# Kernel tuning notes

Measured on AMD Instinct MI355X. Metric: run time of the kernel, lower is better.

The kernel has to match this reference:

```python
import jax, jax.numpy as jnp
import numpy as np

OUT_K = 7  # out_kernel


def setup_inputs() -> dict:
    key = jax.random.key(0)
    k = jax.random.split(key, 12)
    b, cin, h, w = 2, 256, 64, 64
    C, pd = 64, 4          # out_channels, pos_dim
    qc = C - pd            # channels produced by conv_q/k/v
    s = 0.05
    f32 = jnp.float32
    return {
        "x":    jax.random.normal(k[0], (b, cin, h, w), f32),
        "Wq":   jax.random.normal(k[1], (qc, cin), f32) * s,
        "bq":   jax.random.normal(k[2], (qc,), f32) * s,
        "Wk":   jax.random.normal(k[3], (qc, cin), f32) * s,
        "bk":   jax.random.normal(k[4], (qc,), f32) * s,
        "Wv":   jax.random.normal(k[5], (qc, cin), f32) * s,
        "bv":   jax.random.normal(k[6], (qc,), f32) * s,
        "Wp":   jax.random.normal(k[7], (pd, 2), f32) * s,
        "bp":   jax.random.normal(k[8], (pd,), f32) * s,
        "Wout": jax.random.normal(k[9], (C, C, OUT_K, OUT_K), f32) * s,
        "bout": jax.random.normal(k[10], (C,), f32) * s,
    }


def reference(x, Wq, bq, Wk, bk, Wv, bv, Wp, bp, Wout, bout):
    b, cin, h, w = x.shape
    C = Wout.shape[0]  # out_channels
    dt = x.dtype

    # positional encoding: hw_pose is (row_index, col_index) grids -> 1x1 conv to pos_dim chans
    rows = jnp.broadcast_to(jnp.arange(h, dtype=dt)[:, None], (h, w))
    cols = jnp.broadcast_to(jnp.arange(w, dtype=dt)[None, :], (h, w))
    grid = jnp.stack([rows, cols], axis=0)                      # (2,h,w)
    pos = jnp.einsum('oc,chw->ohw', Wp, grid) + bp[:, None, None]  # (pd,h,w)
    pos = jnp.broadcast_to(pos[None], (b,) + pos.shape)         # (b,pd,h,w)

    def conv1x1(W, bias):
        return jnp.einsum('bchw,oc->bohw', x, W) + bias[None, :, None, None]

    qs = jnp.concatenate([conv1x1(Wq, bq), pos], axis=1)        # (b,C,h,w)
    ks = jnp.concatenate([conv1x1(Wk, bk), pos], axis=1)
    vs = jnp.concatenate([conv1x1(Wv, bv), pos], axis=1)

    hw = h * w
    qsf = qs.transpose(0, 2, 3, 1).reshape(b, hw, C)            # (b,hw,C)
    ksf = ks.reshape(b, C, hw)                                  # (b,C,hw)
    vsf = vs.transpose(0, 2, 3, 1)                              # (b,h,w,C)

    qk = jnp.einsum('bnc,bcm->bnm', qsf, ksf) / jnp.sqrt(jnp.asarray(C, dt))
    diag = jnp.arange(hw)
    qk = qk.at[:, diag, diag].set(0.0)                          # zero diagonal BEFORE softmax
    attn = jax.nn.softmax(qk, axis=-1).reshape(b, h, w, h, w)

    # 7x7 clamped neighborhood gather (replaces the 49-iteration python loop)
    r = OUT_K // 2
    offs = jnp.arange(-r, r + 1)
    hi = jnp.clip(jnp.arange(h)[:, None] + offs[None, :], 0, h - 1)  # (h,7)
    wi = jnp.clip(jnp.arange(w)[:, None] + offs[None, :], 0, w - 1)  # (w,7)
    ii = jnp.arange(h)[:, None, None, None]
    jj = jnp.arange(w)[None, :, None, None]
    hk = hi[:, None, :, None]
    wk = wi[None, :, None, :]
    attn_loc = attn[:, ii, jj, hk, wk]                          # (b,h,w,7,7)
    v_loc = vsf[:, hk, wk, :]                                   # (b,h,w,7,7,C)

    qkv = attn_loc[..., None] * v_loc                           # (b,h,w,7,7,C)
    # con_out: kernel=7, stride=7 over a 7x7 patch == full contraction
    out = jnp.einsum('bhwklc,ockl->bhwo', qkv, Wout) + bout     # (b,h,w,C)
    out = jax.nn.relu(out)
    return out.transpose(0, 3, 1, 2)                            # (b,C,h,w)
```

## Files before the change

kernel.cpp:

```cpp
#include <hip/hip_runtime.h>
#include <math.h>

#define NTAP 49

typedef short bf16x8 __attribute__((ext_vector_type(8)));
typedef float f32x4  __attribute__((ext_vector_type(4)));

__device__ __forceinline__ float b2f(ushort u) {
    return __uint_as_float(((unsigned)u) << 16);
}
__device__ __forceinline__ ushort f2b(float f) {
    unsigned u = __float_as_uint(f);
    return (ushort)((u + 0x7FFFu + ((u >> 16) & 1u)) >> 16);
}
__device__ __forceinline__ int iclamp(int x) { return min(max(x, 0), 63); }

#define LOG2E 1.44269504f
#define S2    (0.125f * LOG2E)

#define WTB_OFF 0u
#define WAH_OFF 401408u
#define WAL_OFF 499712u
#define QH_OFF  598016u
#define KH_OFF  1646592u
#define VH_OFF  2695168u
#define LP_OFF  3743744u
#define ST_OFF  4005888u

__global__ __launch_bounds__(256) void k_prep(
    const float* __restrict__ Wout,
    const float* __restrict__ Wq, const float* __restrict__ Wk, const float* __restrict__ Wv,
    ushort* __restrict__ Wtb, ushort* __restrict__ WAh, ushort* __restrict__ WAl,
    int* __restrict__ ST)
{
    int idx = blockIdx.x * 256 + threadIdx.x;
    if (idx < 4) ST[idx] = 0;
    if (idx < 192 * 256) {
        int m = idx >> 8, c = idx & 255;
        int mat = m >> 6, o = m & 63;
        float v = 0.f;
        if (o < 60) {
            const float* Wm = (mat == 0) ? Wq : (mat == 1) ? Wk : Wv;
            v = Wm[o * 256 + c];
        }
        ushort h = f2b(v);
        WAh[idx] = h;
        WAl[idx] = f2b(v - b2f(h));
    }
    if (idx < 64 * 64 * NTAP) {
        int o   = idx / (64 * NTAP);
        int rem = idx - o * (64 * NTAP);
        int c   = rem / NTAP;
        int kl  = rem - c * NTAP;
        Wtb[(o * NTAP + kl) * 64 + c] = f2b(Wout[idx]);
    }
}

__device__ __forceinline__ float get_mhat(const int* ST, int b) {
    float q2 = __int_as_float(ST[b]);
    float k2 = __int_as_float(ST[2 + b]);
    return 0.125f * sqrtf(q2) * sqrtf(k2) + 1.0f;
}

__global__ __launch_bounds__(512, 2) void k_qkv(
    const float* __restrict__ x,
    const ushort* __restrict__ WAh, const ushort* __restrict__ WAl,
    const float* __restrict__ bq, const float* __restrict__ bk, const float* __restrict__ bv,
    const float* __restrict__ Wp, const float* __restrict__ bp,
    ushort* __restrict__ QKV, int* __restrict__ ST)
{
    __shared__ ushort Xh[32 * 256];
    __shared__ ushort Xl[32 * 256];
    __shared__ ushort Wshl[192 * 64];
    __shared__ float  sqL[64];
    int bid = blockIdx.x;
    int b   = bid >> 7;
    int n0  = (bid & 127) * 32;
    int t   = threadIdx.x;
    int w    = t >> 6;
    int L    = t & 63;
    int lrow = L & 15, lk = L >> 4;

    if (t < 64) sqL[t] = 0.f;
    {
        int p  = t & 31;
        int cg = t >> 5;
        #pragma unroll
        for (int it = 0; it < 2; ++it) {
            int cgi = cg + it * 16;
            float v[8];
            #pragma unroll
            for (int e = 0; e < 8; ++e)
                v[e] = x[((size_t)(b * 256 + cgi * 8 + e) << 12) + n0 + p];
            bf16x8 hi, lo;
            #pragma unroll
            for (int e = 0; e < 8; ++e) {
                ushort h = f2b(v[e]);
                hi[e] = (short)h;
                lo[e] = (short)f2b(v[e] - b2f(h));
            }
            int off = p * 256 + ((cgi * 8) ^ ((p & 7) * 8));
            *(bf16x8*)(Xh + off) = hi;
            *(bf16x8*)(Xl + off) = lo;
        }
    }

    int pxh = w >> 2;
    int ob  = (w & 3) * 48;
    int px  = pxh * 16 + lrow;

    f32x4 acc[3] = {{0,0,0,0},{0,0,0,0},{0,0,0,0}};

    for (int c8 = 0; c8 < 8; ++c8) {
        __syncthreads();
        #pragma unroll
        for (int s = 0; s < 3; ++s) {
            int g_idx = t + s * 512;
            int och = g_idx >> 3, g = g_idx & 7;
            const ushort* src = (g < 4) ? WAh : WAl;
            bf16x8 val = *(const bf16x8*)(src + och * 256 + c8 * 32 + (g & 3) * 8);
            *(bf16x8*)((char*)Wshl + och * 128 + ((g * 16) ^ ((och & 7) << 4))) = val;
        }
        __syncthreads();

        int cidx = (c8 * 4 + lk) * 8;
        int o0 = px * 256 + (cidx ^ ((px & 7) * 8));
        bf16x8 ah = *(const bf16x8*)(Xh + o0);
        bf16x8 al = *(const bf16x8*)(Xl + o0);
        #pragma unroll
        for (int c = 0; c < 3; ++c) {
            int och = ob + c * 16 + lrow;
            const char* wb = (const char*)Wshl + och * 128;
            int swz = (och & 7) << 4;
            bf16x8 bh = *(const bf16x8*)(wb + ((lk * 16) ^ swz));
            bf16x8 bl = *(const bf16x8*)(wb + (((4 + lk) * 16) ^ swz));
            acc[c] = __builtin_amdgcn_mfma_f32_16x16x32_bf16(al, bh, acc[c], 0, 0, 0);
            acc[c] = __builtin_amdgcn_mfma_f32_16x16x32_bf16(ah, bl, acc[c], 0, 0, 0);
            acc[c] = __builtin_amdgcn_mfma_f32_16x16x32_bf16(ah, bh, acc[c], 0, 0, 0);
        }
    }

    float s_q[4] = {0,0,0,0}, s_k[4] = {0,0,0,0};
    #pragma unroll
    for (int c = 0; c < 3; ++c) {
        int och = ob + c * 16 + lrow;
        int mat = och >> 6;
        int o   = och & 63;
        const float* bm = (mat == 0) ? bq : (mat == 1) ? bk : bv;
        ushort* Ob = QKV + (size_t)mat * 524288;
        if (o < 60) {
            float bias = bm[o];
            #pragma unroll
            for (int e = 0; e < 4; ++e) {
                int n = n0 + pxh * 16 + lk * 4 + e;
                float v = acc[c][e] + bias;
                Ob[((size_t)((b << 12) + n)) * 64 + o] = f2b(v);
                if (mat == 0) s_q[e] = fmaf(v, v, s_q[e]);
                else if (mat == 1) s_k[e] = fmaf(v, v, s_k[e]);
            }
        } else {
            int po = o - 60;
            float w0 = Wp[2 * po], w1 = Wp[2 * po + 1], b0 = bp[po];
            #pragma unroll
            for (int e = 0; e < 4; ++e) {
                int n = n0 + pxh * 16 + lk * 4 + e;
                float fi = (float)(n >> 6), fj = (float)(n & 63);
                float pv = fmaf(w0, fi, fmaf(w1, fj, b0));
                Ob[((size_t)((b << 12) + n)) * 64 + o] = f2b(pv);
                if (mat == 0) s_q[e] = fmaf(pv, pv, s_q[e]);
                else if (mat == 1) s_k[e] = fmaf(pv, pv, s_k[e]);
            }
        }
    }
    #pragma unroll
    for (int off = 1; off < 16; off <<= 1) {
        #pragma unroll
        for (int e = 0; e < 4; ++e) {
            s_q[e] += __shfl_xor(s_q[e], off, 64);
            s_k[e] += __shfl_xor(s_k[e], off, 64);
        }
    }
    if (lrow == 0) {
        #pragma unroll
        for (int e = 0; e < 4; ++e) {
            int pix = pxh * 16 + lk * 4 + e;
            atomicAdd(&sqL[pix],      s_q[e]);
            atomicAdd(&sqL[32 + pix], s_k[e]);
        }
    }
    __syncthreads();
    if (t < 32) {
        float q2 = sqL[t], k2 = sqL[32 + t];
        #pragma unroll
        for (int off = 1; off < 32; off <<= 1) {
            q2 = fmaxf(q2, __shfl_xor(q2, off, 64));
            k2 = fmaxf(k2, __shfl_xor(k2, off, 64));
        }
        if (t == 0) {
            atomicMax(ST + b,     __float_as_int(q2));
            atomicMax(ST + 2 + b, __float_as_int(k2));
        }
    }
}

__global__ __launch_bounds__(512, 2) void k_stats(
    const ushort* __restrict__ QH, const ushort* __restrict__ KH,
    const int* __restrict__ ST, float* __restrict__ Lp)
{
    __shared__ ushort Ks[2][128 * 64];
    int bid = blockIdx.x;
    int ks  = bid & 7;
    int r   = bid >> 3;
    int b   = r >> 5;
    int n0  = (r & 31) * 128;
    int ck0 = ks * 512;
    float bse = -get_mhat(ST, b) * LOG2E;

    int t = threadIdx.x;
    int w = t >> 6, L = t & 63;
    int lrow = L & 15, lk = L >> 4;

    size_t qbase = ((size_t)((b << 12) + n0 + w * 16 + lrow)) * 64 + lk * 8;
    bf16x8 a0 = *(const bf16x8*)(QH + qbase);
    bf16x8 a1 = *(const bf16x8*)(QH + qbase + 32);

    #pragma unroll
    for (int gi = 0; gi < 2; ++gi) {
        int g = t + gi * 512;
        int u = g >> 3, c8 = g & 7;
        bf16x8 val = *(const bf16x8*)(KH + ((size_t)((b << 12) + ck0 + u)) * 64 + c8 * 8);
        *(bf16x8*)((char*)Ks[0] + u * 128 + ((c8 * 16) ^ ((u & 7) << 4))) = val;
    }

    float rs0 = 0.f, rs1 = 0.f, rs2 = 0.f, rs3 = 0.f;

    for (int c = 0; c < 4; ++c) {
        bf16x8 st0, st1;
        int u0 = t >> 3, c80 = t & 7;
        int u1 = (t + 512) >> 3, c81 = t & 7;
        bool pf = (c + 1) < 4;
        if (pf) {
            st0 = *(const bf16x8*)(KH + ((size_t)((b << 12) + ck0 + (c + 1) * 128 + u0)) * 64 + c80 * 8);
            st1 = *(const bf16x8*)(KH + ((size_t)((b << 12) + ck0 + (c + 1) * 128 + u1)) * 64 + c81 * 8);
        }
        __syncthreads();
        const char* kb = (const char*)Ks[c & 1];
        #pragma unroll
        for (int kg = 0; kg < 8; ++kg) {
            int u = kg * 16 + lrow;
            int swz = (u & 7) << 4;
            bf16x8 b0 = *(const bf16x8*)(kb + u * 128 + ((lk * 16) ^ swz));
            bf16x8 b1 = *(const bf16x8*)(kb + u * 128 + ((64 + lk * 16) ^ swz));
            f32x4 z = {0.f, 0.f, 0.f, 0.f};
            z = __builtin_amdgcn_mfma_f32_16x16x32_bf16(a0, b0, z, 0, 0, 0);
            z = __builtin_amdgcn_mfma_f32_16x16x32_bf16(a1, b1, z, 0, 0, 0);
            rs0 += exp2f(fmaf(z[0], S2, bse));
            rs1 += exp2f(fmaf(z[1], S2, bse));
            rs2 += exp2f(fmaf(z[2], S2, bse));
            rs3 += exp2f(fmaf(z[3], S2, bse));
        }
        if (pf) {
            char* kn = (char*)Ks[(c + 1) & 1];
            *(bf16x8*)(kn + u0 * 128 + ((c80 * 16) ^ ((u0 & 7) << 4))) = st0;
            *(bf16x8*)(kn + u1 * 128 + ((c81 * 16) ^ ((u1 & 7) << 4))) = st1;
        }
    }
    #pragma unroll
    for (int off = 1; off < 16; off <<= 1) {
        rs0 += __shfl_xor(rs0, off, 64);
        rs1 += __shfl_xor(rs1, off, 64);
        rs2 += __shfl_xor(rs2, off, 64);
        rs3 += __shfl_xor(rs3, off, 64);
    }
    if (lrow == 0) {
        float* dst = Lp + ((size_t)(ks * 2 + b) << 12) + n0 + w * 16 + lk * 4;
        dst[0] = rs0; dst[1] = rs1; dst[2] = rs2; dst[3] = rs3;
    }
}

__global__ __launch_bounds__(512, 2) void k_out(
    const ushort* __restrict__ QH, const ushort* __restrict__ KH,
    const ushort* __restrict__ VH, const ushort* __restrict__ Wtb,
    const float* __restrict__ Lp, const int* __restrict__ ST,
    const float* __restrict__ bout, float* __restrict__ out)
{
    __shared__ ushort Vs[7 * 40 * 64];
    __shared__ ushort Kh[7 * 40 * 64];
    __shared__ ushort Ws[7 * 64 * 64];
    __shared__ float  Al2[NTAP * 36];
    __shared__ float  Lrow[32];
    __shared__ float  LcS[32];
    int bid = blockIdx.x;
    int b   = bid >> 7;
    int rem = bid & 127;
    int i   = rem >> 1;
    int j0  = (rem & 1) * 32;
    int n0  = (i << 6) + j0;
    int t   = threadIdx.x;
    int w    = t >> 6;
    int L    = t & 63;
    int lrow = L & 15, lk = L >> 4;
    float bse = -get_mhat(ST, b) * LOG2E;
    float e0  = exp2f(bse);

    for (int g = t; g < 2 * 7 * 38 * 8; g += 512) {
        int which = g >= 7 * 38 * 8;
        int gg = which ? g - 7 * 38 * 8 : g;
        int kk = gg / 304;
        int r2 = gg - kk * 304;
        int u  = r2 >> 3, c8 = r2 & 7;
        int vr = iclamp(i + kk - 3);
        int vc = iclamp(j0 - 3 + u);
        const ushort* src = which ? KH : VH;
        ushort* dst = which ? Kh : Vs;
        bf16x8 val = *(const bf16x8*)(src + ((size_t)((b << 12) + (vr << 6) + vc)) * 64 + c8 * 8);
        *(bf16x8*)((char*)dst + kk * 5120 + u * 128 + ((c8 * 16) ^ ((u & 7) << 4))) = val;
    }
    if (t < 32) {
        int n = n0 + t;
        float s = 0.f;
        #pragma unroll
        for (int ks = 0; ks < 8; ++ks)
            s += Lp[((size_t)(ks * 2 + b) << 12) + n];
        Lrow[t] = s;
    }
    __syncthreads();

    {
        int p = t >> 4, u = t & 15;
        int n = n0 + p;
        int pj = n & 63;
        const ushort* qr = QH + ((size_t)(b << 12) + n) * 64;
        bf16x8 qv[8];
        #pragma unroll
        for (int c8 = 0; c8 < 8; ++c8) qv[c8] = *(const bf16x8*)(qr + c8 * 8);

        int nt = (u == 0) ? 4 : 3;
        float d[4] = {0.f, 0.f, 0.f, 0.f};
        int srcs[4];
        const char* kbp[4];
        int swzs[4];
        #pragma unroll
        for (int m = 0; m < 4; ++m) {
            int tap = (m == 3) ? 48 : (u + 16 * m);
            int kk = tap / 7, ll = tap - kk * 7;
            srcs[m] = (iclamp(i + kk - 3) << 6) + iclamp(pj + ll - 3);
            int uu = p + ll;
            kbp[m]  = (const char*)Kh + kk * 5120 + uu * 128;
            swzs[m] = (uu & 7) << 4;
        }
        #pragma unroll
        for (int c8 = 0; c8 < 8; ++c8) {
            bf16x8 kv0 = *(const bf16x8*)(kbp[0] + ((c8 * 16) ^ swzs[0]));
            bf16x8 kv1 = *(const bf16x8*)(kbp[1] + ((c8 * 16) ^ swzs[1]));
            bf16x8 kv2 = *(const bf16x8*)(kbp[2] + ((c8 * 16) ^ swzs[2]));
            #pragma unroll
            for (int e = 0; e < 8; ++e) {
                float q = b2f((ushort)qv[c8][e]);
                d[0] = fmaf(q, b2f((ushort)kv0[e]), d[0]);
                d[1] = fmaf(q, b2f((ushort)kv1[e]), d[1]);
                d[2] = fmaf(q, b2f((ushort)kv2[e]), d[2]);
            }
        }
        if (nt == 4) {
            #pragma unroll
            for (int c8 = 0; c8 < 8; ++c8) {
                bf16x8 kv3 = *(const bf16x8*)(kbp[3] + ((c8 * 16) ^ swzs[3]));
                #pragma unroll
                for (int e = 0; e < 8; ++e)
                    d[3] = fmaf(b2f((ushort)qv[c8][e]), b2f((ushort)kv3[e]), d[3]);
            }
        }
        if (u == 8)
            LcS[p] = Lrow[p] - exp2f(fmaf(d[1], S2, bse)) + e0;
        __syncthreads();
        float rLc = 1.0f / LcS[p];
        for (int m = 0; m < nt; ++m) {
            int tap = (m == 3) ? 48 : (u + 16 * m);
            float A = (srcs[m] == n) ? (e0 * rLc)
                                     : (exp2f(fmaf(d[m], S2, bse)) * rLc);
            Al2[tap * 36 + p] = A;
        }
    }
    __syncthreads();

    int q16 = (w >> 2) << 4;
    int o16 = (w & 3) << 4;
    int oA  = o16 + lrow;
    int wswz = (oA & 7) << 4;
    f32x4 acc0 = {0.f, 0.f, 0.f, 0.f};

    for (int kk = 0; kk < 7; ++kk) {
        __syncthreads();
        #pragma unroll
        for (int s = 0; s < 7; ++s) {
            int g   = t + s * 512;
            int c8  = g & 7;
            int och = (g >> 3) & 63;
            int ll  = g >> 9;
            bf16x8 val = *(const bf16x8*)(Wtb + ((size_t)(och * NTAP + kk * 7 + ll)) * 64 + c8 * 8);
            *(bf16x8*)((char*)Ws + ll * 8192 + och * 128 + ((c8 * 16) ^ ((och & 7) << 4))) = val;
        }
        __syncthreads();

        const char* vrow = (const char*)Vs + kk * 5120;
        #pragma unroll
        for (int ll = 0; ll < 7; ++ll) {
            int kl = kk * 7 + ll;
            int u = q16 + lrow + ll;
            const char* vb = vrow + u * 128;
            int swz = (u & 7) << 4;
            bf16x8 v0 = *(const bf16x8*)(vb + ((lk * 16) ^ swz));
            bf16x8 v1 = *(const bf16x8*)(vb + ((64 + lk * 16) ^ swz));
            float4 av = *(const float4*)(&Al2[kl * 36 + q16 + lk * 4]);
            const char* wb = (const char*)Ws + ll * 8192 + oA * 128;
            bf16x8 b00 = *(const bf16x8*)(wb + ((lk * 16) ^ wswz));
            bf16x8 b01 = *(const bf16x8*)(wb + (((4 + lk) * 16) ^ wswz));
            f32x4 z = {0.f, 0.f, 0.f, 0.f};
            z = __builtin_amdgcn_mfma_f32_16x16x32_bf16(v0, b00, z, 0, 0, 0);
            z = __builtin_amdgcn_mfma_f32_16x16x32_bf16(v1, b01, z, 0, 0, 0);
            acc0[0] = fmaf(av.x, z[0], acc0[0]);
            acc0[1] = fmaf(av.y, z[1], acc0[1]);
            acc0[2] = fmaf(av.z, z[2], acc0[2]);
            acc0[3] = fmaf(av.w, z[3], acc0[3]);
        }
    }

    int o = oA;
    int nbase = n0 + q16 + lk * 4;
    float bb = bout[o];
    float4 v = make_float4(fmaxf(acc0[0] + bb, 0.f), fmaxf(acc0[1] + bb, 0.f),
                           fmaxf(acc0[2] + bb, 0.f), fmaxf(acc0[3] + bb, 0.f));
    *(float4*)(out + (((size_t)(b * 64 + o)) << 12) + nbase) = v;
}

extern "C" void kernel_launch(void* const* d_in, const int* in_sizes, int n_in,
                              void* d_out, int out_size, void* d_ws, size_t ws_size,
                              hipStream_t stream) {
    const float* x    = (const float*)d_in[0];
    const float* Wq   = (const float*)d_in[1];
    const float* bq   = (const float*)d_in[2];
    const float* Wk   = (const float*)d_in[3];
    const float* bk   = (const float*)d_in[4];
    const float* Wv   = (const float*)d_in[5];
    const float* bv   = (const float*)d_in[6];
    const float* Wp   = (const float*)d_in[7];
    const float* bp   = (const float*)d_in[8];
    const float* Wout = (const float*)d_in[9];
    const float* bout = (const float*)d_in[10];
    float* out = (float*)d_out;

    char* ws = (char*)d_ws;
    ushort* Wtb = (ushort*)(ws + WTB_OFF);
    ushort* WAh = (ushort*)(ws + WAH_OFF);
    ushort* WAl = (ushort*)(ws + WAL_OFF);
    ushort* QKV = (ushort*)(ws + QH_OFF);
    float*  Lp  = (float*)(ws + LP_OFF);
    int*    ST  = (int*)(ws + ST_OFF);

    ushort* QH = QKV;
    ushort* KH = QKV + 524288;
    ushort* VH = QKV + 1048576;

    hipLaunchKernelGGL(k_prep,  dim3(784), dim3(256), 0, stream,
                       Wout, Wq, Wk, Wv, Wtb, WAh, WAl, ST);
    hipLaunchKernelGGL(k_qkv,   dim3(256), dim3(512), 0, stream,
                       x, WAh, WAl, bq, bk, bv, Wp, bp, QKV, ST);
    hipLaunchKernelGGL(k_stats, dim3(512), dim3(512), 0, stream, QH, KH, ST, Lp);
    hipLaunchKernelGGL(k_out,   dim3(256), dim3(512), 0, stream,
                       QH, KH, VH, Wtb, Lp, ST, bout, out);
}
```

Measured before the change: 55.77 us.

## Remove prep kernel, fuse weight conversion into consumers, prefetch weights via registers

Drops the separate k_prep launch. k_qkv now reads the fp32 Wq/Wk/Wv directly and splits them into hi/lo bf16 on the fly, while k_stats converts Wout to the transposed bf16 layout that k_out consumes. The global atomicMax statistics are replaced by per-block max arrays that each consumer block reduces itself, so no zero-initialisation of the counters is needed. Weight tiles in k_qkv and k_out are prefetched into registers one iteration ahead so global loads overlap the MFMA work. The costs are redundant fp32 weight loads and conversions in every k_qkv block, extra register pressure, and an extra reduction per block.

```diff
diff --git a/kernel.cpp b/kernel.cpp
--- a/kernel.cpp
+++ b/kernel.cpp
@@ -19,55 +19,36 @@
 #define S2    (0.125f * LOG2E)
 
 #define WTB_OFF 0u
-#define WAH_OFF 401408u
-#define WAL_OFF 499712u
 #define QH_OFF  598016u
 #define KH_OFF  1646592u
 #define VH_OFF  2695168u
 #define LP_OFF  3743744u
-#define ST_OFF  4005888u
-
-__global__ __launch_bounds__(256) void k_prep(
-    const float* __restrict__ Wout,
-    const float* __restrict__ Wq, const float* __restrict__ Wk, const float* __restrict__ Wv,
-    ushort* __restrict__ Wtb, ushort* __restrict__ WAh, ushort* __restrict__ WAl,
-    int* __restrict__ ST)
-{
-    int idx = blockIdx.x * 256 + threadIdx.x;
-    if (idx < 4) ST[idx] = 0;
-    if (idx < 192 * 256) {
-        int m = idx >> 8, c = idx & 255;
-        int mat = m >> 6, o = m & 63;
-        float v = 0.f;
-        if (o < 60) {
-            const float* Wm = (mat == 0) ? Wq : (mat == 1) ? Wk : Wv;
-            v = Wm[o * 256 + c];
-        }
-        ushort h = f2b(v);
-        WAh[idx] = h;
-        WAl[idx] = f2b(v - b2f(h));
-    }
-    if (idx < 64 * 64 * NTAP) {
-        int o   = idx / (64 * NTAP);
-        int rem = idx - o * (64 * NTAP);
-        int c   = rem / NTAP;
-        int kl  = rem - c * NTAP;
-        Wtb[(o * NTAP + kl) * 64 + c] = f2b(Wout[idx]);
-    }
-}
-
-__device__ __forceinline__ float get_mhat(const int* ST, int b) {
-    float q2 = __int_as_float(ST[b]);
-    float k2 = __int_as_float(ST[2 + b]);
-    return 0.125f * sqrtf(q2) * sqrtf(k2) + 1.0f;
+#define MXQ_OFF 4005888u
+#define MXK_OFF 4006912u
+
+__device__ __forceinline__ float mh_reduce(const float* __restrict__ MXq,
+                                           const float* __restrict__ MXk,
+                                           int b, int t, float* sh) {
+    if (t < 64) {
+        float a = fmaxf(MXq[(b << 7) + t], MXq[(b << 7) + 64 + t]);
+        float k = fmaxf(MXk[(b << 7) + t], MXk[(b << 7) + 64 + t]);
+        #pragma unroll
+        for (int off = 1; off < 64; off <<= 1) {
+            a = fmaxf(a, __shfl_xor(a, off, 64));
+            k = fmaxf(k, __shfl_xor(k, off, 64));
+        }
+        if (t == 0) *sh = 0.125f * sqrtf(a) * sqrtf(k) + 1.0f;
+    }
+    __syncthreads();
+    return *sh;
 }
 
 __global__ __launch_bounds__(512, 2) void k_qkv(
     const float* __restrict__ x,
-    const ushort* __restrict__ WAh, const ushort* __restrict__ WAl,
+    const float* __restrict__ Wq, const float* __restrict__ Wk, const float* __restrict__ Wv,
     const float* __restrict__ bq, const float* __restrict__ bk, const float* __restrict__ bv,
     const float* __restrict__ Wp, const float* __restrict__ bp,
-    ushort* __restrict__ QKV, int* __restrict__ ST)
+    ushort* __restrict__ QKV, float* __restrict__ MXq, float* __restrict__ MXk)
 {
     __shared__ ushort Xh[32 * 256];
     __shared__ ushort Xl[32 * 256];
@@ -105,6 +86,55 @@
         }
     }
 
+    int   s_och[3], s_g[3];
+    bool  s_live[3];
+    const float* s_src[3];
+    #pragma unroll
+    for (int s = 0; s < 3; ++s) {
+        int g_idx = t + s * 512;
+        int och = g_idx >> 3, g = g_idx & 7;
+        int mat = och >> 6, o = och & 63;
+        const float* Wm = (mat == 0) ? Wq : (mat == 1) ? Wk : Wv;
+        s_och[s] = och; s_g[s] = g;
+        s_live[s] = (o < 60);
+        s_src[s] = Wm + o * 256 + (g & 3) * 8;
+    }
+    float4 wreg[3][2];
+
+    #define ISSUE_W(c8) {                                                   \
+        _Pragma("unroll")                                                   \
+        for (int s = 0; s < 3; ++s) {                                       \
+            if (s_live[s]) {                                                \
+                const float* sp = s_src[s] + (c8) * 32;                     \
+                wreg[s][0] = *(const float4*)(sp);                          \
+                wreg[s][1] = *(const float4*)(sp + 4);                      \
+            } else {                                                        \
+                wreg[s][0] = make_float4(0.f,0.f,0.f,0.f);                  \
+                wreg[s][1] = make_float4(0.f,0.f,0.f,0.f);                  \
+            }                                                               \
+        } }
+    #define WRITE_W() {                                                     \
+        _Pragma("unroll")                                                   \
+        for (int s = 0; s < 3; ++s) {                                       \
+            float vv[8] = {wreg[s][0].x, wreg[s][0].y, wreg[s][0].z,        \
+                           wreg[s][0].w, wreg[s][1].x, wreg[s][1].y,        \
+                           wreg[s][1].z, wreg[s][1].w};                     \
+            bf16x8 val;                                                     \
+            _Pragma("unroll")                                               \
+            for (int e = 0; e < 8; ++e) {                                   \
+                ushort h = f2b(vv[e]);                                      \
+                val[e] = (s_g[s] < 4) ? (short)h                            \
+                                      : (short)f2b(vv[e] - b2f(h));         \
+            }                                                               \
+            *(bf16x8*)((char*)Wshl + s_och[s] * 128 +                       \
+                       ((s_g[s] * 16) ^ ((s_och[s] & 7) << 4))) = val;      \
+        } }
+
+    ISSUE_W(0);
+    __syncthreads();
+    WRITE_W();
+    __syncthreads();
+
     int pxh = w >> 2;
     int ob  = (w & 3) * 48;
     int px  = pxh * 16 + lrow;
@@ -112,17 +142,7 @@
     f32x4 acc[3] = {{0,0,0,0},{0,0,0,0},{0,0,0,0}};
 
     for (int c8 = 0; c8 < 8; ++c8) {
-        __syncthreads();
-        #pragma unroll
-        for (int s = 0; s < 3; ++s) {
-            int g_idx = t + s * 512;
-            int och = g_idx >> 3, g = g_idx & 7;
-            const ushort* src = (g < 4) ? WAh : WAl;
-            bf16x8 val = *(const bf16x8*)(src + och * 256 + c8 * 32 + (g & 3) * 8);
-            *(bf16x8*)((char*)Wshl + och * 128 + ((g * 16) ^ ((och & 7) << 4))) = val;
-        }
-        __syncthreads();
-
+        if (c8 + 1 < 8) ISSUE_W(c8 + 1);
         int cidx = (c8 * 4 + lk) * 8;
         int o0 = px * 256 + (cidx ^ ((px & 7) * 8));
         bf16x8 ah = *(const bf16x8*)(Xh + o0);
@@ -138,6 +158,9 @@
             acc[c] = __builtin_amdgcn_mfma_f32_16x16x32_bf16(ah, bl, acc[c], 0, 0, 0);
             acc[c] = __builtin_amdgcn_mfma_f32_16x16x32_bf16(ah, bh, acc[c], 0, 0, 0);
         }
+        __syncthreads();
+        if (c8 + 1 < 8) WRITE_W();
+        __syncthreads();
     }
 
     float s_q[4] = {0,0,0,0}, s_k[4] = {0,0,0,0};
@@ -196,27 +219,38 @@
             q2 = fmaxf(q2, __shfl_xor(q2, off, 64));
             k2 = fmaxf(k2, __shfl_xor(k2, off, 64));
         }
-        if (t == 0) {
-            atomicMax(ST + b,     __float_as_int(q2));
-            atomicMax(ST + 2 + b, __float_as_int(k2));
-        }
+        if (t == 0) { MXq[bid] = q2; MXk[bid] = k2; }
     }
 }
 
 __global__ __launch_bounds__(512, 2) void k_stats(
+    const float* __restrict__ Wout, ushort* __restrict__ Wtb,
     const ushort* __restrict__ QH, const ushort* __restrict__ KH,
-    const int* __restrict__ ST, float* __restrict__ Lp)
+    const float* __restrict__ MXq, const float* __restrict__ MXk,
+    float* __restrict__ Lp)
 {
     __shared__ ushort Ks[2][128 * 64];
+    __shared__ float  mhs;
     int bid = blockIdx.x;
     int ks  = bid & 7;
     int r   = bid >> 3;
     int b   = r >> 5;
     int n0  = (r & 31) * 128;
     int ck0 = ks * 512;
-    float bse = -get_mhat(ST, b) * LOG2E;
-
     int t = threadIdx.x;
+
+    {
+        int widx = bid * 512 + t;
+        if (widx < 64 * 64 * NTAP) {
+            int o   = widx / (64 * NTAP);
+            int rem = widx - o * (64 * NTAP);
+            int c   = rem / NTAP;
+            int kl  = rem - c * NTAP;
+            Wtb[(o * NTAP + kl) * 64 + c] = f2b(Wout[widx]);
+        }
+    }
+    float bse = -mh_reduce(MXq, MXk, b, t, &mhs) * LOG2E;
+
     int w = t >> 6, L = t & 63;
     int lrow = L & 15, lk = L >> 4;
 
@@ -281,7 +315,8 @@
 __global__ __launch_bounds__(512, 2) void k_out(
     const ushort* __restrict__ QH, const ushort* __restrict__ KH,
     const ushort* __restrict__ VH, const ushort* __restrict__ Wtb,
-    const float* __restrict__ Lp, const int* __restrict__ ST,
+    const float* __restrict__ Lp,
+    const float* __restrict__ MXq, const float* __restrict__ MXk,
     const float* __restrict__ bout, float* __restrict__ out)
 {
     __shared__ ushort Vs[7 * 40 * 64];
@@ -290,6 +325,7 @@
     __shared__ float  Al2[NTAP * 36];
     __shared__ float  Lrow[32];
     __shared__ float  LcS[32];
+    __shared__ float  mhs;
     int bid = blockIdx.x;
     int b   = bid >> 7;
     int rem = bid & 127;
@@ -300,8 +336,26 @@
     int w    = t >> 6;
     int L    = t & 63;
     int lrow = L & 15, lk = L >> 4;
-    float bse = -get_mhat(ST, b) * LOG2E;
+
+    float bse = -mh_reduce(MXq, MXk, b, t, &mhs) * LOG2E;
     float e0  = exp2f(bse);
+
+    bf16x8 wreg[7];
+    #define ISSUE_WS(kk) {                                                          \
+        _Pragma("unroll")                                                           \
+        for (int s = 0; s < 7; ++s) {                                               \
+            int g = t + s * 512;                                                    \
+            int c8 = g & 7, och = (g >> 3) & 63, ll = g >> 9;                       \
+            wreg[s] = *(const bf16x8*)(Wtb + ((size_t)(och * NTAP + (kk) * 7 + ll)) * 64 + c8 * 8); \
+        } }
+    #define WRITE_WS() {                                                            \
+        _Pragma("unroll")                                                           \
+        for (int s = 0; s < 7; ++s) {                                               \
+            int g = t + s * 512;                                                    \
+            int c8 = g & 7, och = (g >> 3) & 63, ll = g >> 9;                       \
+            *(bf16x8*)((char*)Ws + ll * 8192 + och * 128 +                          \
+                       ((c8 * 16) ^ ((och & 7) << 4))) = wreg[s];                   \
+        } }
 
     for (int g = t; g < 2 * 7 * 38 * 8; g += 512) {
         int which = g >= 7 * 38 * 8;
@@ -316,6 +370,8 @@
         bf16x8 val = *(const bf16x8*)(src + ((size_t)((b << 12) + (vr << 6) + vc)) * 64 + c8 * 8);
         *(bf16x8*)((char*)dst + kk * 5120 + u * 128 + ((c8 * 16) ^ ((u & 7) << 4))) = val;
     }
+    ISSUE_WS(0);
+    WRITE_WS();
     if (t < 32) {
         int n = n0 + t;
         float s = 0.f;
@@ -391,18 +447,7 @@
     f32x4 acc0 = {0.f, 0.f, 0.f, 0.f};
 
     for (int kk = 0; kk < 7; ++kk) {
-        __syncthreads();
-        #pragma unroll
-        for (int s = 0; s < 7; ++s) {
-            int g   = t + s * 512;
-            int c8  = g & 7;
-            int och = (g >> 3) & 63;
-            int ll  = g >> 9;
-            bf16x8 val = *(const bf16x8*)(Wtb + ((size_t)(och * NTAP + kk * 7 + ll)) * 64 + c8 * 8);
-            *(bf16x8*)((char*)Ws + ll * 8192 + och * 128 + ((c8 * 16) ^ ((och & 7) << 4))) = val;
-        }
-        __syncthreads();
-
+        if (kk + 1 < 7) ISSUE_WS(kk + 1);
         const char* vrow = (const char*)Vs + kk * 5120;
         #pragma unroll
         for (int ll = 0; ll < 7; ++ll) {
@@ -424,6 +469,9 @@
             acc0[2] = fmaf(av.z, z[2], acc0[2]);
             acc0[3] = fmaf(av.w, z[3], acc0[3]);
         }
+        __syncthreads();
+        if (kk + 1 < 7) WRITE_WS();
+        __syncthreads();
     }
 
     int o = oA;
@@ -452,21 +500,19 @@
 
     char* ws = (char*)d_ws;
     ushort* Wtb = (ushort*)(ws + WTB_OFF);
-    ushort* WAh = (ushort*)(ws + WAH_OFF);
-    ushort* WAl = (ushort*)(ws + WAL_OFF);
     ushort* QKV = (ushort*)(ws + QH_OFF);
     float*  Lp  = (float*)(ws + LP_OFF);
-    int*    ST  = (int*)(ws + ST_OFF);
+    float*  MXq = (float*)(ws + MXQ_OFF);
+    float*  MXk = (float*)(ws + MXK_OFF);
 
     ushort* QH = QKV;
     ushort* KH = QKV + 524288;
     ushort* VH = QKV + 1048576;
 
-    hipLaunchKernelGGL(k_prep,  dim3(784), dim3(256), 0, stream,
-                       Wout, Wq, Wk, Wv, Wtb, WAh, WAl, ST);
     hipLaunchKernelGGL(k_qkv,   dim3(256), dim3(512), 0, stream,
-                       x, WAh, WAl, bq, bk, bv, Wp, bp, QKV, ST);
-    hipLaunchKernelGGL(k_stats, dim3(512), dim3(512), 0, stream, QH, KH, ST, Lp);
+                       x, Wq, Wk, Wv, bq, bk, bv, Wp, bp, QKV, MXq, MXk);
+    hipLaunchKernelGGL(k_stats, dim3(512), dim3(512), 0, stream,
+                       Wout, Wtb, QH, KH, MXq, MXk, Lp);
     hipLaunchKernelGGL(k_out,   dim3(256), dim3(512), 0, stream,
-                       QH, KH, VH, Wtb, Lp, ST, bout, out);
-}
+                       QH, KH, VH, Wtb, Lp, MXq, MXk, bout, out);
+}
```

Result: faster. 50.54 us (-9.4%).
